# Kernel optimization log

Hardware: AMD Instinct MI355X
Metric: run time of the kernel (lower is better)

Reference implementation:

```python
import jax, jax.numpy as jnp
import numpy as np

ALPHA = 0.2  # LeakyReLU negative slope
NEG_INF = -9e15


def setup_inputs() -> dict:
    key = jax.random.key(0)
    k1, k2, k3, k4 = jax.random.split(key, 4)
    B, S, N, F_in, F_out = 4, 8, 1024, 128, 64
    inputs = jax.random.normal(k1, (B, S, N, F_in), dtype=jnp.float32)
    Adj = jax.random.randint(k2, (B, S, N, N), 0, 2, dtype=jnp.int32)
    # xavier_normal_ with gain=1.414
    W = jax.random.normal(k3, (F_in, F_out), dtype=jnp.float32) * np.float32(1.414 * np.sqrt(2.0 / (F_in + F_out)))
    a = jax.random.normal(k4, (2 * F_out, 1), dtype=jnp.float32) * np.float32(1.414 * np.sqrt(2.0 / (2 * F_out + 1)))
    return {"inputs": inputs, "Adj": Adj, "W": W, "a": a}


def reference(inputs, Adj, W, a):
    h = jnp.einsum('bsnf,fo->bsno', inputs, W)  # [B,S,N,F_out]
    F_out = h.shape[-1]
    # additive score e_ij = leakyrelu(a1.h_i + a2.h_j); identical math to the
    # original concat([h_i, h_j]) @ a without the O(N^2 * 2F) tensor.
    a1 = a[:F_out, 0]
    a2 = a[F_out:, 0]
    f1 = h @ a1  # [B,S,N]
    f2 = h @ a2  # [B,S,N]
    e = jax.nn.leaky_relu(f1[..., :, None] + f2[..., None, :], ALPHA)  # [B,S,N,N]
    att = jnp.where(Adj > 0, e, jnp.float32(NEG_INF))
    att = jax.nn.softmax(att, axis=1)  # faithful to original: softmax over dim=1 (SEQ)
    # dropout omitted (p=0.0 / eval mode)
    h_prime = jnp.matmul(att, h)  # [B,S,N,F_out]
    return jax.nn.elu(h_prime), Adj  # concat=True branch
```

## Files before the change

### kernel.cpp

```cpp
#include <hip/hip_runtime.h>
#include <cstdint>
#include <cstddef>

#define LALPHA 0.2f
#define NEG_INF -9000000000000000.0f

constexpr int N_ = 1024;
constexpr int FIN = 128, FO = 64;
constexpr int BS = 32;
constexpr size_t H_ELEMS = (size_t)BS * N_ * FO;
constexpr size_t F_ELEMS = (size_t)BS * N_;
constexpr int SPLITK = 8;

typedef __attribute__((ext_vector_type(8))) short short8;
typedef __attribute__((ext_vector_type(4))) float floatx4;
typedef __attribute__((ext_vector_type(4))) int   i32x4;
typedef __attribute__((ext_vector_type(4))) unsigned u32x4;

static __device__ __forceinline__ unsigned short f2bf(float x) {
    union { float f; unsigned u; } v; v.f = x;
    unsigned r = v.u + 0x7FFF + ((v.u >> 16) & 1);
    return (unsigned short)(r >> 16);
}
static __device__ __forceinline__ float bf2f_lo(unsigned u) {
    union { unsigned u; float f; } v; v.u = u << 16; return v.f;
}
static __device__ __forceinline__ float bf2f_hi(unsigned u) {
    union { unsigned u; float f; } v; v.u = u & 0xFFFF0000u; return v.f;
}

__global__ __launch_bounds__(256) void k_h(
    const float* __restrict__ x, const float* __restrict__ W,
    const float* __restrict__ a, float* __restrict__ h,
    float* __restrict__ f1, float* __restrict__ f2)
{
    __shared__ float sW[FIN * FO];
    __shared__ float sx[4][FIN];
    const int t = threadIdx.x;
    for (int i = t; i < FIN * FO; i += 256) sW[i] = W[i];
    const size_t node0 = (size_t)blockIdx.x * 4;
    for (int i = t; i < 4 * FIN; i += 256) sx[i >> 7][i & 127] = x[node0 * FIN + i];
    __syncthreads();

    const int wave = t >> 6;
    const int lane = t & 63;
    const size_t node = node0 + wave;

    float acc = 0.f;
    #pragma unroll
    for (int f = 0; f < FIN; ++f)
        acc = fmaf(sx[wave][f], sW[f * FO + lane], acc);

    h[node * FO + lane] = acc;

    float v1 = acc * a[lane];
    float v2 = acc * a[FO + lane];
    #pragma unroll
    for (int off = 32; off > 0; off >>= 1) {
        v1 += __shfl_xor(v1, off);
        v2 += __shfl_xor(v2, off);
    }
    if (lane == 0) { f1[node] = v1; f2[node] = v2; }
}

__global__ __launch_bounds__(256) void k_tr(
    const float* __restrict__ h, unsigned short* __restrict__ hT)
{
    __shared__ float lt[64][65];
    const int bs = blockIdx.x >> 4;
    const int n0 = (blockIdx.x & 15) * 64;
    const int t = threadIdx.x;
    const float* hb = h + ((size_t)bs << 16) + ((size_t)n0 << 6);
    #pragma unroll
    for (int k = 0; k < 4; ++k) {
        const int r = (t >> 4) + k * 16;
        const int c = (t & 15) * 4;
        const float4 v = *(const float4*)(hb + ((size_t)r << 6) + c);
        lt[r][c] = v.x; lt[r][c + 1] = v.y; lt[r][c + 2] = v.z; lt[r][c + 3] = v.w;
    }
    __syncthreads();
    const int o = t >> 2, ch = (t & 3) * 16;
    unsigned short tmp[16];
    #pragma unroll
    for (int q = 0; q < 16; ++q) tmp[q] = f2bf(lt[ch + q][o]);
    unsigned short* dst = hT + ((size_t)bs << 16) + ((size_t)o << 10) + n0 + ch;
    *(uint4*)dst = *(uint4*)tmp;
    *(uint4*)(dst + 8) = *(uint4*)(tmp + 8);
}

__global__ __launch_bounds__(256) void k_pack(
    const int* __restrict__ Adj, float* __restrict__ adjf,
    unsigned char* __restrict__ packed)
{
    const size_t tid = (size_t)blockIdx.x * 256 + threadIdx.x;
    const int j4 = (int)(tid & 255) * 4;
    const int i  = (int)((tid >> 8) & 1023);
    const int b  = (int)(tid >> 18);

    unsigned b0 = 0, b1 = 0, b2 = 0, b3 = 0;
    #pragma unroll
    for (int s = 0; s < 8; ++s) {
        const size_t off = ((size_t)(b * 8 + s) << 20) + ((size_t)i << 10) + (size_t)j4;
        const i32x4 ad = __builtin_nontemporal_load((const i32x4*)(Adj + off));
        floatx4 o;
        o.x = (float)ad.x; o.y = (float)ad.y; o.z = (float)ad.z; o.w = (float)ad.w;
        __builtin_nontemporal_store(o, (floatx4*)(adjf + off));
        b0 |= (unsigned)(ad.x > 0) << s;
        b1 |= (unsigned)(ad.y > 0) << s;
        b2 |= (unsigned)(ad.z > 0) << s;
        b3 |= (unsigned)(ad.w > 0) << s;
    }
    uchar4 pk;
    pk.x = (unsigned char)b0; pk.y = (unsigned char)b1;
    pk.z = (unsigned char)b2; pk.w = (unsigned char)b3;
    *(uchar4*)(packed + ((size_t)b << 20) + ((size_t)i << 10) + (size_t)j4) = pk;
}

__global__ __launch_bounds__(256, 4) void k_av(
    const unsigned char* __restrict__ packed, const float* __restrict__ f1,
    const float* __restrict__ f2, const unsigned short* __restrict__ hT,
    unsigned short* __restrict__ part)
{
    __shared__ __align__(16) unsigned short att[2][8][16][64];

    const int bid   = blockIdx.x;
    const int kk    = bid >> 8;
    const int b     = (bid >> 6) & 3;
    const int i0    = (bid & 63) * 16;
    const int t     = threadIdx.x;

    const int p_jj = (t & 15) * 4;
    const int p_ii = t >> 4;
    const int gi   = i0 + p_ii;

    const int w  = t >> 6;
    const int l  = t & 63;
    const int fr = l & 15;
    const int fg = l >> 4;

    float fi[8];
    #pragma unroll
    for (int s = 0; s < 8; ++s) fi[s] = f1[(size_t)(b * 8 + s) * N_ + gi];

    floatx4 acc[2][4];
    #pragma unroll
    for (int si = 0; si < 2; ++si)
        #pragma unroll
        for (int n = 0; n < 4; ++n)
            acc[si][n] = (floatx4){0.f, 0.f, 0.f, 0.f};

    auto compute_att = [&](int jt, int pb) {
        const int j0 = (kk * 2 + jt) * 64;
        const uchar4 pk = *(const uchar4*)(
            packed + ((size_t)b << 20) + ((size_t)gi << 10) + (size_t)(j0 + p_jj));
        const unsigned bq0 = pk.x, bq1 = pk.y, bq2 = pk.z, bq3 = pk.w;

        float ev[8][4];
        #pragma unroll
        for (int s = 0; s < 8; ++s) {
            const float4 fj = *(const float4*)(f2 + (size_t)(b * 8 + s) * N_ + j0 + p_jj);
            const float v0 = fi[s] + fj.x, v1 = fi[s] + fj.y;
            const float v2 = fi[s] + fj.z, v3 = fi[s] + fj.w;
            ev[s][0] = (bq0 >> s) & 1 ? (v0 >= 0.f ? v0 : LALPHA * v0) : NEG_INF;
            ev[s][1] = (bq1 >> s) & 1 ? (v1 >= 0.f ? v1 : LALPHA * v1) : NEG_INF;
            ev[s][2] = (bq2 >> s) & 1 ? (v2 >= 0.f ? v2 : LALPHA * v2) : NEG_INF;
            ev[s][3] = (bq3 >> s) & 1 ? (v3 >= 0.f ? v3 : LALPHA * v3) : NEG_INF;
        }
        #pragma unroll
        for (int q = 0; q < 4; ++q) {
            float m = NEG_INF;
            #pragma unroll
            for (int s = 0; s < 8; ++s) m = fmaxf(m, ev[s][q]);
            float p[8], den = 0.f;
            #pragma unroll
            for (int s = 0; s < 8; ++s) { p[s] = __expf(ev[s][q] - m); den += p[s]; }
            const float r = 1.0f / den;
            #pragma unroll
            for (int s = 0; s < 8; ++s) ev[s][q] = p[s] * r;
        }
        const int chs  = (p_jj >> 3) ^ (p_ii & 7);
        const int boff = chs * 16 + (p_jj & 7) * 2;
        #pragma unroll
        for (int s = 0; s < 8; ++s) {
            ushort4 wv;
            wv.x = f2bf(ev[s][0]); wv.y = f2bf(ev[s][1]);
            wv.z = f2bf(ev[s][2]); wv.w = f2bf(ev[s][3]);
            *(ushort4*)((char*)&att[pb][s][p_ii][0] + boff) = wv;
        }
    };

    auto do_mfma = [&](int jt, int pb) {
        const int j0 = (kk * 2 + jt) * 64;
        #pragma unroll
        for (int ks = 0; ks < 2; ++ks) {
            short8 af[2];
            #pragma unroll
            for (int si = 0; si < 2; ++si) {
                const int s = 2 * w + si;
                const int c = (ks * 4 + fg) ^ (fr & 7);
                af[si] = *(const short8*)((const char*)&att[pb][s][fr][0] + c * 16);
            }
            #pragma unroll
            for (int n = 0; n < 4; ++n) {
                #pragma unroll
                for (int si = 0; si < 2; ++si) {
                    const int bs = b * 8 + 2 * w + si;
                    const short8 bf = *(const short8*)(
                        hT + ((size_t)bs << 16) + (size_t)(n * 16 + fr) * N_ + j0 + ks * 32 + fg * 8);
                    acc[si][n] = __builtin_amdgcn_mfma_f32_16x16x32_bf16(af[si], bf, acc[si][n], 0, 0, 0);
                }
            }
        }
    };

    compute_att(0, 0);
    __syncthreads();
    compute_att(1, 1);
    do_mfma(0, 0);
    __syncthreads();
    do_mfma(1, 1);

    #pragma unroll
    for (int si = 0; si < 2; ++si) {
        const int bs = b * 8 + 2 * w + si;
        #pragma unroll
        for (int n = 0; n < 4; ++n) {
            #pragma unroll
            for (int r = 0; r < 4; ++r) {
                __builtin_nontemporal_store(f2bf(acc[si][n][r]),
                    part + (size_t)kk * H_ELEMS + ((size_t)bs << 16)
                         + (size_t)(i0 + fg * 4 + r) * FO + n * 16 + fr);
            }
        }
    }
}

__global__ __launch_bounds__(256) void k_comb(
    const unsigned short* __restrict__ part, float* __restrict__ out_h)
{
    const size_t idx = ((size_t)blockIdx.x * 256 + threadIdx.x) * 8;
    float acc[8] = {0.f,0.f,0.f,0.f,0.f,0.f,0.f,0.f};
    #pragma unroll
    for (int p = 0; p < SPLITK; ++p) {
        const u32x4 v = __builtin_nontemporal_load(
            (const u32x4*)(part + (size_t)p * H_ELEMS + idx));
        acc[0] += bf2f_lo(v.x); acc[1] += bf2f_hi(v.x);
        acc[2] += bf2f_lo(v.y); acc[3] += bf2f_hi(v.y);
        acc[4] += bf2f_lo(v.z); acc[5] += bf2f_hi(v.z);
        acc[6] += bf2f_lo(v.w); acc[7] += bf2f_hi(v.w);
    }
    floatx4 r0, r1;
    r0.x = acc[0] > 0.f ? acc[0] : expm1f(acc[0]);
    r0.y = acc[1] > 0.f ? acc[1] : expm1f(acc[1]);
    r0.z = acc[2] > 0.f ? acc[2] : expm1f(acc[2]);
    r0.w = acc[3] > 0.f ? acc[3] : expm1f(acc[3]);
    r1.x = acc[4] > 0.f ? acc[4] : expm1f(acc[4]);
    r1.y = acc[5] > 0.f ? acc[5] : expm1f(acc[5]);
    r1.z = acc[6] > 0.f ? acc[6] : expm1f(acc[6]);
    r1.w = acc[7] > 0.f ? acc[7] : expm1f(acc[7]);
    __builtin_nontemporal_store(r0, (floatx4*)(out_h + idx));
    __builtin_nontemporal_store(r1, (floatx4*)(out_h + idx + 4));
}

extern "C" void kernel_launch(void* const* d_in, const int* in_sizes, int n_in,
                              void* d_out, int out_size, void* d_ws, size_t ws_size,
                              hipStream_t stream)
{
    const float* x   = (const float*)d_in[0];
    const int*   Adj = (const int*)d_in[1];
    const float* W   = (const float*)d_in[2];
    const float* a   = (const float*)d_in[3];

    float* out = (float*)d_out;
    float* ws  = (float*)d_ws;

    float* f1 = ws;
    float* f2 = f1 + F_ELEMS;
    unsigned short* hT = (unsigned short*)(f2 + F_ELEMS);
    unsigned char* packed = (unsigned char*)(hT + H_ELEMS);
    float* h = (float*)(packed + (size_t)4 * 1024 * 1024);
    unsigned short* part = (unsigned short*)h;

    float* out_h   = out;
    float* out_adj = out + H_ELEMS;

    hipLaunchKernelGGL(k_h,    dim3(BS * N_ / 4),           dim3(256), 0, stream, x, W, a, h, f1, f2);
    hipLaunchKernelGGL(k_tr,   dim3(BS * 16),               dim3(256), 0, stream, h, hT);
    hipLaunchKernelGGL(k_pack, dim3(4096),                  dim3(256), 0, stream, Adj, out_adj, packed);
    hipLaunchKernelGGL(k_av,   dim3(SPLITK * 4 * 64),       dim3(256), 0, stream, packed, f1, f2, hT, part);
    hipLaunchKernelGGL(k_comb, dim3((int)(H_ELEMS / 2048)), dim3(256), 0, stream, part, out_h);
}
```

Measured before the change: 155.6 us.

## Precompute softmax log-sum-exp in the Adj pass and reuse it in the attention kernel

The adjacency packing kernel now also computes the masked leaky-ReLU scores and stores a per-(b,i,j) log-sum-exp over the sequence axis. The attention kernel then forms each probability as a single exp(e - lse) instead of running a max/exp/sum/divide per element. All-masked columns are handled by writing a uniform 1/8. MFMA sections are also wrapped in raised wave priority. The cost is an extra 16 MB float write and read of the LSE buffer, plus f1/f2 reads in the front kernel, in exchange for lighter ALU work in k_av.

```diff
diff --git a/kernel.cpp b/kernel.cpp
--- a/kernel.cpp
+++ b/kernel.cpp
@@ -10,6 +10,7 @@
 constexpr int BS = 32;
 constexpr size_t H_ELEMS = (size_t)BS * N_ * FO;
 constexpr size_t F_ELEMS = (size_t)BS * N_;
+constexpr size_t M_ELEMS = (size_t)4 * N_ * N_;
 constexpr int SPLITK = 8;
 
 typedef __attribute__((ext_vector_type(8))) short short8;
@@ -88,38 +89,70 @@
     *(uint4*)(dst + 8) = *(uint4*)(tmp + 8);
 }
 
-__global__ __launch_bounds__(256) void k_pack(
-    const int* __restrict__ Adj, float* __restrict__ adjf,
-    unsigned char* __restrict__ packed)
+__global__ __launch_bounds__(256) void k_front(
+    const int* __restrict__ Adj, const float* __restrict__ f1,
+    const float* __restrict__ f2, float* __restrict__ adjf,
+    unsigned char* __restrict__ packed, float* __restrict__ mld)
 {
     const size_t tid = (size_t)blockIdx.x * 256 + threadIdx.x;
     const int j4 = (int)(tid & 255) * 4;
     const int i  = (int)((tid >> 8) & 1023);
     const int b  = (int)(tid >> 18);
 
-    unsigned b0 = 0, b1 = 0, b2 = 0, b3 = 0;
+    i32x4 ad[8];
     #pragma unroll
     for (int s = 0; s < 8; ++s) {
         const size_t off = ((size_t)(b * 8 + s) << 20) + ((size_t)i << 10) + (size_t)j4;
-        const i32x4 ad = __builtin_nontemporal_load((const i32x4*)(Adj + off));
+        ad[s] = __builtin_nontemporal_load((const i32x4*)(Adj + off));
+    }
+    float fi[8];
+    #pragma unroll
+    for (int s = 0; s < 8; ++s) fi[s] = f1[(size_t)(b * 8 + s) * N_ + i];
+
+    float ev[8][4];
+    unsigned b0 = 0, b1 = 0, b2 = 0, b3 = 0;
+    #pragma unroll
+    for (int s = 0; s < 8; ++s) {
+        const size_t off = ((size_t)(b * 8 + s) << 20) + ((size_t)i << 10) + (size_t)j4;
         floatx4 o;
-        o.x = (float)ad.x; o.y = (float)ad.y; o.z = (float)ad.z; o.w = (float)ad.w;
+        o.x = (float)ad[s].x; o.y = (float)ad[s].y;
+        o.z = (float)ad[s].z; o.w = (float)ad[s].w;
         __builtin_nontemporal_store(o, (floatx4*)(adjf + off));
-        b0 |= (unsigned)(ad.x > 0) << s;
-        b1 |= (unsigned)(ad.y > 0) << s;
-        b2 |= (unsigned)(ad.z > 0) << s;
-        b3 |= (unsigned)(ad.w > 0) << s;
-    }
+        const float4 fj = *(const float4*)(f2 + (size_t)(b * 8 + s) * N_ + j4);
+        const float v0 = fi[s] + fj.x, v1 = fi[s] + fj.y;
+        const float v2 = fi[s] + fj.z, v3 = fi[s] + fj.w;
+        ev[s][0] = ad[s].x > 0 ? (v0 >= 0.f ? v0 : LALPHA * v0) : NEG_INF;
+        ev[s][1] = ad[s].y > 0 ? (v1 >= 0.f ? v1 : LALPHA * v1) : NEG_INF;
+        ev[s][2] = ad[s].z > 0 ? (v2 >= 0.f ? v2 : LALPHA * v2) : NEG_INF;
+        ev[s][3] = ad[s].w > 0 ? (v3 >= 0.f ? v3 : LALPHA * v3) : NEG_INF;
+        b0 |= (unsigned)(ad[s].x > 0) << s;
+        b1 |= (unsigned)(ad[s].y > 0) << s;
+        b2 |= (unsigned)(ad[s].z > 0) << s;
+        b3 |= (unsigned)(ad[s].w > 0) << s;
+    }
+    floatx4 ml;
+    #pragma unroll
+    for (int q = 0; q < 4; ++q) {
+        float m = NEG_INF;
+        #pragma unroll
+        for (int s = 0; s < 8; ++s) m = fmaxf(m, ev[s][q]);
+        float den = 0.f;
+        #pragma unroll
+        for (int s = 0; s < 8; ++s) den += __expf(ev[s][q] - m);
+        ml[q] = m + __logf(den);
+    }
+    const size_t moff = ((size_t)b << 20) + ((size_t)i << 10) + (size_t)j4;
+    __builtin_nontemporal_store(ml, (floatx4*)(mld + moff));
     uchar4 pk;
     pk.x = (unsigned char)b0; pk.y = (unsigned char)b1;
     pk.z = (unsigned char)b2; pk.w = (unsigned char)b3;
-    *(uchar4*)(packed + ((size_t)b << 20) + ((size_t)i << 10) + (size_t)j4) = pk;
+    *(uchar4*)(packed + moff) = pk;
 }
 
 __global__ __launch_bounds__(256, 4) void k_av(
     const unsigned char* __restrict__ packed, const float* __restrict__ f1,
-    const float* __restrict__ f2, const unsigned short* __restrict__ hT,
-    unsigned short* __restrict__ part)
+    const float* __restrict__ f2, const float* __restrict__ mld,
+    const unsigned short* __restrict__ hT, unsigned short* __restrict__ part)
 {
     __shared__ __align__(16) unsigned short att[2][8][16][64];
 
@@ -151,8 +184,9 @@
 
     auto compute_att = [&](int jt, int pb) {
         const int j0 = (kk * 2 + jt) * 64;
-        const uchar4 pk = *(const uchar4*)(
-            packed + ((size_t)b << 20) + ((size_t)gi << 10) + (size_t)(j0 + p_jj));
+        const size_t moff = ((size_t)b << 20) + ((size_t)gi << 10) + (size_t)(j0 + p_jj);
+        const uchar4 pk = *(const uchar4*)(packed + moff);
+        const float4 md = *(const float4*)(mld + moff);
         const unsigned bq0 = pk.x, bq1 = pk.y, bq2 = pk.z, bq3 = pk.w;
 
         float ev[8][4];
@@ -161,22 +195,14 @@
             const float4 fj = *(const float4*)(f2 + (size_t)(b * 8 + s) * N_ + j0 + p_jj);
             const float v0 = fi[s] + fj.x, v1 = fi[s] + fj.y;
             const float v2 = fi[s] + fj.z, v3 = fi[s] + fj.w;
-            ev[s][0] = (bq0 >> s) & 1 ? (v0 >= 0.f ? v0 : LALPHA * v0) : NEG_INF;
-            ev[s][1] = (bq1 >> s) & 1 ? (v1 >= 0.f ? v1 : LALPHA * v1) : NEG_INF;
-            ev[s][2] = (bq2 >> s) & 1 ? (v2 >= 0.f ? v2 : LALPHA * v2) : NEG_INF;
-            ev[s][3] = (bq3 >> s) & 1 ? (v3 >= 0.f ? v3 : LALPHA * v3) : NEG_INF;
-        }
-        #pragma unroll
-        for (int q = 0; q < 4; ++q) {
-            float m = NEG_INF;
-            #pragma unroll
-            for (int s = 0; s < 8; ++s) m = fmaxf(m, ev[s][q]);
-            float p[8], den = 0.f;
-            #pragma unroll
-            for (int s = 0; s < 8; ++s) { p[s] = __expf(ev[s][q] - m); den += p[s]; }
-            const float r = 1.0f / den;
-            #pragma unroll
-            for (int s = 0; s < 8; ++s) ev[s][q] = p[s] * r;
+            const float e0 = (bq0 >> s) & 1 ? (v0 >= 0.f ? v0 : LALPHA * v0) : NEG_INF;
+            const float e1 = (bq1 >> s) & 1 ? (v1 >= 0.f ? v1 : LALPHA * v1) : NEG_INF;
+            const float e2 = (bq2 >> s) & 1 ? (v2 >= 0.f ? v2 : LALPHA * v2) : NEG_INF;
+            const float e3 = (bq3 >> s) & 1 ? (v3 >= 0.f ? v3 : LALPHA * v3) : NEG_INF;
+            ev[s][0] = bq0 ? __expf(e0 - md.x) : 0.125f;
+            ev[s][1] = bq1 ? __expf(e1 - md.y) : 0.125f;
+            ev[s][2] = bq2 ? __expf(e2 - md.z) : 0.125f;
+            ev[s][3] = bq3 ? __expf(e3 - md.w) : 0.125f;
         }
         const int chs  = (p_jj >> 3) ^ (p_ii & 7);
         const int boff = chs * 16 + (p_jj & 7) * 2;
@@ -191,6 +217,7 @@
 
     auto do_mfma = [&](int jt, int pb) {
         const int j0 = (kk * 2 + jt) * 64;
+        __builtin_amdgcn_s_setprio(1);
         #pragma unroll
         for (int ks = 0; ks < 2; ++ks) {
             short8 af[2];
@@ -211,6 +238,7 @@
                 }
             }
         }
+        __builtin_amdgcn_s_setprio(0);
     };
 
     compute_att(0, 0);
@@ -278,15 +306,16 @@
     float* f2 = f1 + F_ELEMS;
     unsigned short* hT = (unsigned short*)(f2 + F_ELEMS);
     unsigned char* packed = (unsigned char*)(hT + H_ELEMS);
-    float* h = (float*)(packed + (size_t)4 * 1024 * 1024);
-    unsigned short* part = (unsigned short*)h;
+    float* mld = (float*)(packed + M_ELEMS);
+    float* h   = mld + M_ELEMS;
+    unsigned short* part = (unsigned short*)(h + H_ELEMS);
 
     float* out_h   = out;
     float* out_adj = out + H_ELEMS;
 
-    hipLaunchKernelGGL(k_h,    dim3(BS * N_ / 4),           dim3(256), 0, stream, x, W, a, h, f1, f2);
-    hipLaunchKernelGGL(k_tr,   dim3(BS * 16),               dim3(256), 0, stream, h, hT);
-    hipLaunchKernelGGL(k_pack, dim3(4096),                  dim3(256), 0, stream, Adj, out_adj, packed);
-    hipLaunchKernelGGL(k_av,   dim3(SPLITK * 4 * 64),       dim3(256), 0, stream, packed, f1, f2, hT, part);
-    hipLaunchKernelGGL(k_comb, dim3((int)(H_ELEMS / 2048)), dim3(256), 0, stream, part, out_h);
-}
+    hipLaunchKernelGGL(k_h,     dim3(BS * N_ / 4),           dim3(256), 0, stream, x, W, a, h, f1, f2);
+    hipLaunchKernelGGL(k_tr,    dim3(BS * 16),               dim3(256), 0, stream, h, hT);
+    hipLaunchKernelGGL(k_front, dim3(4096),                  dim3(256), 0, stream, Adj, f1, f2, out_adj, packed, mld);
+    hipLaunchKernelGGL(k_av,    dim3(SPLITK * 4 * 64),       dim3(256), 0, stream, packed, f1, f2, mld, hT, part);
+    hipLaunchKernelGGL(k_comb,  dim3((int)(H_ELEMS / 2048)), dim3(256), 0, stream, part, out_h);
+}
```

Result: slower. 169.1 us (+8.7%).
